# Kernel optimization log

Hardware: AMD Instinct MI355X
Metric: run time of the kernel (lower is better)

## Reference

```python
import jax, jax.numpy as jnp
import numpy as np
from jax import lax

NUM_HEADS = 8
HEAD_DIM = 32
DIM = NUM_HEADS * HEAD_DIM  # 256
SR = 2
B, H, W = 4, 64, 64


def setup_inputs() -> dict:
    key = jax.random.key(0)
    ks = jax.random.split(key, 6)
    x = jax.random.normal(ks[0], (B, DIM, H, W), dtype=jnp.float32)
    # query: 1x1 conv without bias -> plain [out,in] matrix
    Wq = jax.random.normal(ks[1], (DIM, DIM), dtype=jnp.float32) * (1.0 / np.sqrt(DIM))
    # key/value: sr x sr conv, stride sr, no bias (OIHW)
    Wk = jax.random.normal(ks[2], (DIM, DIM, SR, SR), dtype=jnp.float32) * (1.0 / np.sqrt(DIM * SR * SR))
    Wv = jax.random.normal(ks[3], (DIM, DIM, SR, SR), dtype=jnp.float32) * (1.0 / np.sqrt(DIM * SR * SR))
    rel_h = jax.random.normal(ks[4], (1, NUM_HEADS, HEAD_DIM, 1, H // SR), dtype=jnp.float32)
    rel_w = jax.random.normal(ks[5], (1, NUM_HEADS, HEAD_DIM, W // SR, 1), dtype=jnp.float32)
    return {"x": x, "Wq": Wq, "Wk": Wk, "Wv": Wv, "rel_h": rel_h, "rel_w": rel_w}


def reference(x, Wq, Wk, Wv, rel_h, rel_w):
    b, c, h, w = x.shape
    nh, hd = NUM_HEADS, HEAD_DIM
    scale = hd ** (-0.5)
    dn = ('NCHW', 'OIHW', 'NCHW')

    # q: 1x1 conv == channel matmul; [B, C, H*W] -> [B, nh, hd, Nq]
    q = jnp.einsum('oc,bchw->bohw', Wq, x).reshape(b, nh, hd, h * w)
    # k, v: sr x sr conv, stride sr -> [B, nh, hd, Nkv]
    k = lax.conv_general_dilated(x, Wk, window_strides=(SR, SR), padding='VALID',
                                 dimension_numbers=dn).reshape(b, nh, hd, -1)
    v = lax.conv_general_dilated(x, Wv, window_strides=(SR, SR), padding='VALID',
                                 dimension_numbers=dn).reshape(b, nh, hd, -1)

    # attn scores: q^T k -> [B, nh, Nq, Nkv]
    attn = jnp.einsum('bhdn,bhdm->bhnm', q, k)
    # relative positional bias: (rel_h + rel_w) broadcast -> [nh, hd, Nkv]
    pos = (rel_h + rel_w).reshape(nh, hd, -1)
    attn = attn + jnp.einsum('bhdn,hdm->bhnm', q, pos)
    attn = jax.nn.softmax(attn * scale, axis=-1)

    # out = v @ attn^T -> [B, nh, hd, Nq] -> [B, C, H, W]
    out = jnp.einsum('bhdm,bhnm->bhdn', v, attn).reshape(b, c, h, w)
    return out
```

## Files before the change

kernel.cpp:

```cpp
#include <hip/hip_runtime.h>
#include <math.h>


typedef __bf16 bf16;
typedef __attribute__((ext_vector_type(8))) __bf16 bf16x8;
typedef __attribute__((ext_vector_type(4))) float f32x4;
typedef __attribute__((ext_vector_type(4))) _Float16 f16x4;

#define MFMA16 __builtin_amdgcn_mfma_f32_16x16x32_bf16
#define MFMA16H __builtin_amdgcn_mfma_f32_16x16x16f16

#define QSCALE 0.25503486f
#define SOFTMAX_SHIFT 10.0f

__global__ void k_prep_w(const float* __restrict__ Wq, const float* __restrict__ Wk,
                         const float* __restrict__ Wv,
                         bf16* __restrict__ Wq_bf, bf16* __restrict__ Wkv_bf) {
    int idx = blockIdx.x * 256 + threadIdx.x;
    Wq_bf[idx] = (bf16)(Wq[idx] * QSCALE);
#pragma unroll
    for (int r = 0; r < 8; r++) {
        int e = idx + r * 65536;
        int c = e >> 10, kk = e & 1023;
        int tap = kk >> 8, i = kk & 255;
        const float* Wsrc = (c < 256) ? Wk : Wv;
        int cs = c & 255;
        Wkv_bf[e] = (bf16)Wsrc[(cs * 256 + i) * 4 + tap];
    }
}

__global__ void k_xT(const float* __restrict__ x, bf16* __restrict__ xT) {
    int b = blockIdx.z, c0 = blockIdx.y * 64, n0 = blockIdx.x * 64;
    __shared__ float tile[64][65];
    int t = threadIdx.x;
    const float* xp = x + (size_t)(b * 256 + c0) * 4096 + n0;
#pragma unroll
    for (int k2 = 0; k2 < 16; k2++) {
        int flat = k2 * 256 + t;
        int row = flat >> 6, col = flat & 63;
        tile[row][col] = xp[(size_t)row * 4096 + col];
    }
    __syncthreads();
    bf16* op = xT + (size_t)(b * 4096 + n0) * 256 + c0;
#pragma unroll
    for (int k2 = 0; k2 < 16; k2++) {
        int flat = k2 * 256 + t;
        int row = flat >> 6, col = flat & 63;
        op[(size_t)row * 256 + col] = (bf16)tile[col][row];
    }
}

__launch_bounds__(256)
__global__ void k_gemm_q(const bf16* __restrict__ xT, const bf16* __restrict__ Wq_bf,
                         bf16* __restrict__ q_t) {
    int b = blockIdx.z;
    int n0 = blockIdx.x * 64, c0 = blockIdx.y * 64;
    int t = threadIdx.x, l = t & 63, w = t >> 6;
    int wn = (w & 1) * 32, wc = (w >> 1) * 32;
    int lr = l & 15, lg = l >> 4;
    const bf16* Ab = xT + (size_t)(b * 4096 + n0 + wn + lr) * 256 + lg * 8;
    const bf16* Bb = Wq_bf + (size_t)(c0 + wc + lr) * 256 + lg * 8;
    f32x4 acc[2][2] = {};
#pragma unroll
    for (int kk = 0; kk < 8; kk++) {
        bf16x8 a0 = *(const bf16x8*)(Ab + kk * 32);
        bf16x8 a1 = *(const bf16x8*)(Ab + 16 * 256 + kk * 32);
        bf16x8 b0 = *(const bf16x8*)(Bb + kk * 32);
        bf16x8 b1 = *(const bf16x8*)(Bb + 16 * 256 + kk * 32);
        acc[0][0] = MFMA16(a0, b0, acc[0][0], 0, 0, 0);
        acc[0][1] = MFMA16(a0, b1, acc[0][1], 0, 0, 0);
        acc[1][0] = MFMA16(a1, b0, acc[1][0], 0, 0, 0);
        acc[1][1] = MFMA16(a1, b1, acc[1][1], 0, 0, 0);
    }
#pragma unroll
    for (int i = 0; i < 2; i++)
#pragma unroll
        for (int j = 0; j < 2; j++) {
            int cc = c0 + wc + j * 16 + lr;
            int h = cc >> 5, d = cc & 31;
#pragma unroll
            for (int r = 0; r < 4; r++) {
                int n = n0 + wn + i * 16 + lg * 4 + r;
                q_t[((size_t)(b * 8 + h) * 4096 + n) * 32 + d] = (bf16)acc[i][j][r];
            }
        }
}

__device__ inline void p_row_ptrs(const bf16* __restrict__ xb, int m, int lgofs,
                                  const bf16* __restrict__ p[4]) {
    int y = m >> 5, xw = m & 31;
    int nb = y * 128 + xw * 2;
#pragma unroll
    for (int tap = 0; tap < 4; tap++) {
        int n = nb + (tap >> 1) * 64 + (tap & 1);
        p[tap] = xb + (size_t)n * 256 + lgofs;
    }
}
__device__ inline void c_row_ptrs(const bf16* __restrict__ row, int lgofs,
                                  const bf16* __restrict__ p[4]) {
#pragma unroll
    for (int tap = 0; tap < 4; tap++) p[tap] = row + tap * 256 + lgofs;
}

__launch_bounds__(256)
__global__ void k_gemm_kv(const bf16* __restrict__ xT, const bf16* __restrict__ Wkv_bf,
                          const float* __restrict__ rel_h, const float* __restrict__ rel_w,
                          bf16* __restrict__ kpos_t, _Float16* __restrict__ v_td) {
    int b = blockIdx.z;
    int m0 = blockIdx.x * 64;
    int zz = blockIdx.y;
    bool vmode = zz >= 4;
    int c0 = (zz & 3) * 64;
    int t = threadIdx.x, l = t & 63, w = t >> 6;
    int wr = (w & 1) * 32, wc = (w >> 1) * 32;
    int lr = l & 15, lg = l >> 4;
    int lgofs = lg * 8;
    const bf16* xb = xT + (size_t)b * 4096 * 256;
    const bf16 *A0[4], *A1[4], *B0[4], *B1[4];
    if (!vmode) {
        p_row_ptrs(xb, m0 + wr + lr, lgofs, A0);
        p_row_ptrs(xb, m0 + wr + 16 + lr, lgofs, A1);
        c_row_ptrs(Wkv_bf + (size_t)(c0 + wc + lr) * 1024, lgofs, B0);
        c_row_ptrs(Wkv_bf + (size_t)(c0 + wc + 16 + lr) * 1024, lgofs, B1);
    } else {
        c_row_ptrs(Wkv_bf + (size_t)(256 + c0 + wr + lr) * 1024, lgofs, A0);
        c_row_ptrs(Wkv_bf + (size_t)(256 + c0 + wr + 16 + lr) * 1024, lgofs, A1);
        p_row_ptrs(xb, m0 + wc + lr, lgofs, B0);
        p_row_ptrs(xb, m0 + wc + 16 + lr, lgofs, B1);
    }
    f32x4 acc[2][2] = {};
#pragma unroll
    for (int tap = 0; tap < 4; tap++) {
#pragma unroll
        for (int j = 0; j < 8; j++) {
            int o = j * 32;
            bf16x8 a0 = *(const bf16x8*)(A0[tap] + o);
            bf16x8 a1 = *(const bf16x8*)(A1[tap] + o);
            bf16x8 b0 = *(const bf16x8*)(B0[tap] + o);
            bf16x8 b1 = *(const bf16x8*)(B1[tap] + o);
            acc[0][0] = MFMA16(a0, b0, acc[0][0], 0, 0, 0);
            acc[0][1] = MFMA16(a0, b1, acc[0][1], 0, 0, 0);
            acc[1][0] = MFMA16(a1, b0, acc[1][0], 0, 0, 0);
            acc[1][1] = MFMA16(a1, b1, acc[1][1], 0, 0, 0);
        }
    }
    if (!vmode) {
#pragma unroll
        for (int i = 0; i < 2; i++)
#pragma unroll
            for (int j = 0; j < 2; j++) {
                int cc = c0 + wc + j * 16 + lr;
#pragma unroll
                for (int r = 0; r < 4; r++) {
                    int m = m0 + wr + i * 16 + lg * 4 + r;
                    float val = acc[i][j][r] + rel_w[cc * 32 + (m >> 5)]
                                            + rel_h[cc * 32 + (m & 31)];
                    kpos_t[((size_t)(b * 8 + (cc >> 5)) * 1024 + m) * 32 + (cc & 31)] = (bf16)val;
                }
            }
    } else {
#pragma unroll
        for (int i = 0; i < 2; i++)
#pragma unroll
            for (int j = 0; j < 2; j++) {
                int m = m0 + wc + j * 16 + lr;
#pragma unroll
                for (int r = 0; r < 4; r++) {
                    int cc = c0 + wr + i * 16 + lg * 4 + r;
                    v_td[((size_t)(b * 8 + (cc >> 5)) * 32 + (cc & 31)) * 1024 + m] = (_Float16)acc[i][j][r];
                }
            }
    }
}

__launch_bounds__(256)
__global__ void k_attn(const bf16* __restrict__ q_t, const bf16* __restrict__ kpos_t,
                       const _Float16* __restrict__ v_td, float* __restrict__ out) {
    int b = blockIdx.z, h = blockIdx.y;
    int t = threadIdx.x;
    int w = t >> 6, l = t & 63;
    int n0 = blockIdx.x * 128 + w * 32;
    int lr = l & 15, lg = l >> 4;
    const size_t bh = (size_t)(b * 8 + h);
    __shared__ __align__(16) bf16 Ks[256 * 32];
    __shared__ __align__(16) _Float16 Vs[32][264];
    bf16x8 bq0 = *(const bf16x8*)(q_t + (bh * 4096 + n0 + lr) * 32 + lg * 8);
    bf16x8 bq1 = *(const bf16x8*)(q_t + (bh * 4096 + n0 + 16 + lr) * 32 + lg * 8);
    const bf16* Kb = kpos_t + bh * 1024 * 32;
    const _Float16* Vb = v_td + bh * 32 * 1024;
    f32x4 accO[2][2] = {};
    float ps0 = 0.f, ps1 = 0.f;
    const f32x4 zs = {-SOFTMAX_SHIFT, -SOFTMAX_SHIFT, -SOFTMAX_SHIFT, -SOFTMAX_SHIFT};
    for (int pass = 0; pass < 4; pass++) {
        const uint4* ksrc = (const uint4*)(Kb + (size_t)pass * 256 * 32);
        uint4* kdst = (uint4*)Ks;
#pragma unroll
        for (int j = 0; j < 4; j++) kdst[t + j * 256] = ksrc[t + j * 256];
#pragma unroll
        for (int j = 0; j < 4; j++) {
            int u = t + j * 256;
            int row = u >> 5, col = u & 31;
            *(uint4*)(&Vs[row][col * 8]) =
                *(const uint4*)(Vb + (size_t)row * 1024 + pass * 256 + col * 8);
        }
        __syncthreads();
#pragma unroll 4
        for (int tt = 0; tt < 16; tt++) {
            bf16x8 ak = *(const bf16x8*)(Ks + (tt * 16 + lr) * 32 + lg * 8);
            f32x4 s0 = MFMA16(ak, bq0, zs, 0, 0, 0);
            f32x4 s1 = MFMA16(ak, bq1, zs, 0, 0, 0);
            f16x4 p0, p1;
#pragma unroll
            for (int r = 0; r < 4; r++) {
                float e0 = fminf(__builtin_amdgcn_exp2f(s0[r]), 65504.f);
                float e1 = fminf(__builtin_amdgcn_exp2f(s1[r]), 65504.f);
                ps0 += e0; ps1 += e1;
                p0[r] = (_Float16)e0; p1[r] = (_Float16)e1;
            }
            f16x4 v0 = *(const f16x4*)(&Vs[lr][tt * 16 + lg * 4]);
            f16x4 v1 = *(const f16x4*)(&Vs[16 + lr][tt * 16 + lg * 4]);
            accO[0][0] = MFMA16H(p0, v0, accO[0][0], 0, 0, 0);
            accO[0][1] = MFMA16H(p0, v1, accO[0][1], 0, 0, 0);
            accO[1][0] = MFMA16H(p1, v0, accO[1][0], 0, 0, 0);
            accO[1][1] = MFMA16H(p1, v1, accO[1][1], 0, 0, 0);
        }
        __syncthreads();
    }
    ps0 += __shfl_xor(ps0, 16, 64); ps0 += __shfl_xor(ps0, 32, 64);
    ps1 += __shfl_xor(ps1, 16, 64); ps1 += __shfl_xor(ps1, 32, 64);
    float inv0[4], inv1[4];
#pragma unroll
    for (int r = 0; r < 4; r++) {
        inv0[r] = 1.0f / __shfl(ps0, lg * 4 + r, 64);
        inv1[r] = 1.0f / __shfl(ps1, lg * 4 + r, 64);
    }
#pragma unroll
    for (int dt = 0; dt < 2; dt++) {
        int c = h * 32 + dt * 16 + lr;
        float* op0 = out + (size_t)(b * 256 + c) * 4096 + n0 + lg * 4;
        float* op1 = op0 + 16;
        f32x4 o0, o1;
#pragma unroll
        for (int r = 0; r < 4; r++) {
            o0[r] = accO[0][dt][r] * inv0[r];
            o1[r] = accO[1][dt][r] * inv1[r];
        }
        *(f32x4*)op0 = o0;
        *(f32x4*)op1 = o1;
    }
}

extern "C" void kernel_launch(void* const* d_in, const int* in_sizes, int n_in,
                              void* d_out, int out_size, void* d_ws, size_t ws_size,
                              hipStream_t stream) {
    const float* x    = (const float*)d_in[0];
    const float* Wq   = (const float*)d_in[1];
    const float* Wk   = (const float*)d_in[2];
    const float* Wv   = (const float*)d_in[3];
    const float* relh = (const float*)d_in[4];
    const float* relw = (const float*)d_in[5];
    float* out = (float*)d_out;
    char* ws = (char*)d_ws;

    bf16*      xT     = (bf16*)(ws);
    bf16*      q_t    = (bf16*)(ws + (8u << 20));
    bf16*      kposT  = (bf16*)(ws + (16u << 20));
    _Float16*  v_td   = (_Float16*)(ws + (18u << 20));
    bf16*      Wq_bf  = (bf16*)(ws + (20u << 20));
    bf16*      Wkv_bf = (bf16*)(ws + (20u << 20) + (256u << 10));

    k_prep_w <<<256,            256, 0, stream>>>(Wq, Wk, Wv, Wq_bf, Wkv_bf);
    k_xT     <<<dim3(64, 4, 4), 256, 0, stream>>>(x, xT);
    k_gemm_q <<<dim3(64, 4, 4), 256, 0, stream>>>(xT, Wq_bf, q_t);
    k_gemm_kv<<<dim3(16, 8, 4), 256, 0, stream>>>(xT, Wkv_bf, relh, relw, kposT, v_td);
    k_attn   <<<dim3(32, 8, 4), 256, 0, stream>>>(q_t, kposT, v_td, out);
}
```

Before: 170.0 us.

## Fuse Q projection into attention kernel and shrink KV GEMM tiles

```diff
diff --git a/kernel.cpp b/kernel.cpp
--- a/kernel.cpp
+++ b/kernel.cpp
@@ -50,42 +50,6 @@
     }
 }
 
-__launch_bounds__(256)
-__global__ void k_gemm_q(const bf16* __restrict__ xT, const bf16* __restrict__ Wq_bf,
-                         bf16* __restrict__ q_t) {
-    int b = blockIdx.z;
-    int n0 = blockIdx.x * 64, c0 = blockIdx.y * 64;
-    int t = threadIdx.x, l = t & 63, w = t >> 6;
-    int wn = (w & 1) * 32, wc = (w >> 1) * 32;
-    int lr = l & 15, lg = l >> 4;
-    const bf16* Ab = xT + (size_t)(b * 4096 + n0 + wn + lr) * 256 + lg * 8;
-    const bf16* Bb = Wq_bf + (size_t)(c0 + wc + lr) * 256 + lg * 8;
-    f32x4 acc[2][2] = {};
-#pragma unroll
-    for (int kk = 0; kk < 8; kk++) {
-        bf16x8 a0 = *(const bf16x8*)(Ab + kk * 32);
-        bf16x8 a1 = *(const bf16x8*)(Ab + 16 * 256 + kk * 32);
-        bf16x8 b0 = *(const bf16x8*)(Bb + kk * 32);
-        bf16x8 b1 = *(const bf16x8*)(Bb + 16 * 256 + kk * 32);
-        acc[0][0] = MFMA16(a0, b0, acc[0][0], 0, 0, 0);
-        acc[0][1] = MFMA16(a0, b1, acc[0][1], 0, 0, 0);
-        acc[1][0] = MFMA16(a1, b0, acc[1][0], 0, 0, 0);
-        acc[1][1] = MFMA16(a1, b1, acc[1][1], 0, 0, 0);
-    }
-#pragma unroll
-    for (int i = 0; i < 2; i++)
-#pragma unroll
-        for (int j = 0; j < 2; j++) {
-            int cc = c0 + wc + j * 16 + lr;
-            int h = cc >> 5, d = cc & 31;
-#pragma unroll
-            for (int r = 0; r < 4; r++) {
-                int n = n0 + wn + i * 16 + lg * 4 + r;
-                q_t[((size_t)(b * 8 + h) * 4096 + n) * 32 + d] = (bf16)acc[i][j][r];
-            }
-        }
-}
-
 __device__ inline void p_row_ptrs(const bf16* __restrict__ xb, int m, int lgofs,
                                   const bf16* __restrict__ p[4]) {
     int y = m >> 5, xw = m & 31;
@@ -107,75 +71,75 @@
                           const float* __restrict__ rel_h, const float* __restrict__ rel_w,
                           bf16* __restrict__ kpos_t, _Float16* __restrict__ v_td) {
     int b = blockIdx.z;
-    int m0 = blockIdx.x * 64;
+    int m0 = blockIdx.x * 32;
     int zz = blockIdx.y;
     bool vmode = zz >= 4;
     int c0 = (zz & 3) * 64;
     int t = threadIdx.x, l = t & 63, w = t >> 6;
-    int wr = (w & 1) * 32, wc = (w >> 1) * 32;
     int lr = l & 15, lg = l >> 4;
     int lgofs = lg * 8;
     const bf16* xb = xT + (size_t)b * 4096 * 256;
-    const bf16 *A0[4], *A1[4], *B0[4], *B1[4];
+    const bf16 *F0[4], *F1[4], *G0[4];
     if (!vmode) {
-        p_row_ptrs(xb, m0 + wr + lr, lgofs, A0);
-        p_row_ptrs(xb, m0 + wr + 16 + lr, lgofs, A1);
-        c_row_ptrs(Wkv_bf + (size_t)(c0 + wc + lr) * 1024, lgofs, B0);
-        c_row_ptrs(Wkv_bf + (size_t)(c0 + wc + 16 + lr) * 1024, lgofs, B1);
+        p_row_ptrs(xb, m0 + lr, lgofs, F0);
+        p_row_ptrs(xb, m0 + 16 + lr, lgofs, F1);
+        c_row_ptrs(Wkv_bf + (size_t)(c0 + w * 16 + lr) * 1024, lgofs, G0);
     } else {
-        c_row_ptrs(Wkv_bf + (size_t)(256 + c0 + wr + lr) * 1024, lgofs, A0);
-        c_row_ptrs(Wkv_bf + (size_t)(256 + c0 + wr + 16 + lr) * 1024, lgofs, A1);
-        p_row_ptrs(xb, m0 + wc + lr, lgofs, B0);
-        p_row_ptrs(xb, m0 + wc + 16 + lr, lgofs, B1);
-    }
-    f32x4 acc[2][2] = {};
-#pragma unroll
-    for (int tap = 0; tap < 4; tap++) {
-#pragma unroll
-        for (int j = 0; j < 8; j++) {
-            int o = j * 32;
-            bf16x8 a0 = *(const bf16x8*)(A0[tap] + o);
-            bf16x8 a1 = *(const bf16x8*)(A1[tap] + o);
-            bf16x8 b0 = *(const bf16x8*)(B0[tap] + o);
-            bf16x8 b1 = *(const bf16x8*)(B1[tap] + o);
-            acc[0][0] = MFMA16(a0, b0, acc[0][0], 0, 0, 0);
-            acc[0][1] = MFMA16(a0, b1, acc[0][1], 0, 0, 0);
-            acc[1][0] = MFMA16(a1, b0, acc[1][0], 0, 0, 0);
-            acc[1][1] = MFMA16(a1, b1, acc[1][1], 0, 0, 0);
-        }
-    }
+        c_row_ptrs(Wkv_bf + (size_t)(256 + c0 + w * 16 + lr) * 1024, lgofs, G0);
+        p_row_ptrs(xb, m0 + lr, lgofs, F0);
+        p_row_ptrs(xb, m0 + 16 + lr, lgofs, F1);
+    }
+    f32x4 acc[2] = {};
     if (!vmode) {
 #pragma unroll
+        for (int tap = 0; tap < 4; tap++)
+#pragma unroll
+            for (int j = 0; j < 8; j++) {
+                int o = j * 32;
+                bf16x8 a0 = *(const bf16x8*)(F0[tap] + o);
+                bf16x8 a1 = *(const bf16x8*)(F1[tap] + o);
+                bf16x8 b0 = *(const bf16x8*)(G0[tap] + o);
+                acc[0] = MFMA16(a0, b0, acc[0], 0, 0, 0);
+                acc[1] = MFMA16(a1, b0, acc[1], 0, 0, 0);
+            }
+        int cc = c0 + w * 16 + lr;
+#pragma unroll
         for (int i = 0; i < 2; i++)
 #pragma unroll
-            for (int j = 0; j < 2; j++) {
-                int cc = c0 + wc + j * 16 + lr;
-#pragma unroll
-                for (int r = 0; r < 4; r++) {
-                    int m = m0 + wr + i * 16 + lg * 4 + r;
-                    float val = acc[i][j][r] + rel_w[cc * 32 + (m >> 5)]
-                                            + rel_h[cc * 32 + (m & 31)];
-                    kpos_t[((size_t)(b * 8 + (cc >> 5)) * 1024 + m) * 32 + (cc & 31)] = (bf16)val;
-                }
+            for (int r = 0; r < 4; r++) {
+                int m = m0 + i * 16 + lg * 4 + r;
+                float val = acc[i][r] + rel_w[cc * 32 + (m >> 5)]
+                                      + rel_h[cc * 32 + (m & 31)];
+                kpos_t[((size_t)(b * 8 + (cc >> 5)) * 1024 + m) * 32 + (cc & 31)] = (bf16)val;
             }
     } else {
 #pragma unroll
-        for (int i = 0; i < 2; i++)
-#pragma unroll
-            for (int j = 0; j < 2; j++) {
-                int m = m0 + wc + j * 16 + lr;
-#pragma unroll
-                for (int r = 0; r < 4; r++) {
-                    int cc = c0 + wr + i * 16 + lg * 4 + r;
-                    v_td[((size_t)(b * 8 + (cc >> 5)) * 32 + (cc & 31)) * 1024 + m] = (_Float16)acc[i][j][r];
-                }
-            }
+        for (int tap = 0; tap < 4; tap++)
+#pragma unroll
+            for (int j = 0; j < 8; j++) {
+                int o = j * 32;
+                bf16x8 a0 = *(const bf16x8*)(G0[tap] + o);
+                bf16x8 b0 = *(const bf16x8*)(F0[tap] + o);
+                bf16x8 b1 = *(const bf16x8*)(F1[tap] + o);
+                acc[0] = MFMA16(a0, b0, acc[0], 0, 0, 0);
+                acc[1] = MFMA16(a0, b1, acc[1], 0, 0, 0);
+            }
+#pragma unroll
+        for (int j = 0; j < 2; j++) {
+            int m = m0 + j * 16 + lr;
+#pragma unroll
+            for (int r = 0; r < 4; r++) {
+                int cc = c0 + w * 16 + lg * 4 + r;
+                v_td[((size_t)(b * 8 + (cc >> 5)) * 32 + (cc & 31)) * 1024 + m] = (_Float16)acc[j][r];
+            }
+        }
     }
 }
 
 __launch_bounds__(256)
-__global__ void k_attn(const bf16* __restrict__ q_t, const bf16* __restrict__ kpos_t,
-                       const _Float16* __restrict__ v_td, float* __restrict__ out) {
+__global__ void k_attn(const bf16* __restrict__ xT, const bf16* __restrict__ Wq_bf,
+                       const bf16* __restrict__ kpos_t, const _Float16* __restrict__ v_td,
+                       float* __restrict__ out) {
     int b = blockIdx.z, h = blockIdx.y;
     int t = threadIdx.x;
     int w = t >> 6, l = t & 63;
@@ -184,8 +148,33 @@
     const size_t bh = (size_t)(b * 8 + h);
     __shared__ __align__(16) bf16 Ks[256 * 32];
     __shared__ __align__(16) _Float16 Vs[32][264];
-    bf16x8 bq0 = *(const bf16x8*)(q_t + (bh * 4096 + n0 + lr) * 32 + lg * 8);
-    bf16x8 bq1 = *(const bf16x8*)(q_t + (bh * 4096 + n0 + 16 + lr) * 32 + lg * 8);
+    bf16* Qs = Ks + w * 1024;
+    {
+        const bf16* Aw = Wq_bf + (size_t)(h * 32 + lr) * 256 + lg * 8;
+        const bf16* Bx = xT + (size_t)(b * 4096 + n0 + lr) * 256 + lg * 8;
+        f32x4 aq[2][2] = {};
+#pragma unroll
+        for (int kk = 0; kk < 8; kk++) {
+            bf16x8 a0 = *(const bf16x8*)(Aw + kk * 32);
+            bf16x8 a1 = *(const bf16x8*)(Aw + 16 * 256 + kk * 32);
+            bf16x8 b0 = *(const bf16x8*)(Bx + kk * 32);
+            bf16x8 b1 = *(const bf16x8*)(Bx + 16 * 256 + kk * 32);
+            aq[0][0] = MFMA16(a0, b0, aq[0][0], 0, 0, 0);
+            aq[0][1] = MFMA16(a0, b1, aq[0][1], 0, 0, 0);
+            aq[1][0] = MFMA16(a1, b0, aq[1][0], 0, 0, 0);
+            aq[1][1] = MFMA16(a1, b1, aq[1][1], 0, 0, 0);
+        }
+#pragma unroll
+        for (int i = 0; i < 2; i++)
+#pragma unroll
+            for (int j = 0; j < 2; j++)
+#pragma unroll
+                for (int r = 0; r < 4; r++)
+                    Qs[(j * 16 + lr) * 32 + i * 16 + lg * 4 + r] = (bf16)aq[i][j][r];
+    }
+    bf16x8 bq0 = *(const bf16x8*)(Qs + lr * 32 + lg * 8);
+    bf16x8 bq1 = *(const bf16x8*)(Qs + (16 + lr) * 32 + lg * 8);
+    __syncthreads();
     const bf16* Kb = kpos_t + bh * 1024 * 32;
     const _Float16* Vb = v_td + bh * 32 * 1024;
     f32x4 accO[2][2] = {};
@@ -263,15 +252,13 @@
     char* ws = (char*)d_ws;
 
     bf16*      xT     = (bf16*)(ws);
-    bf16*      q_t    = (bf16*)(ws + (8u << 20));
-    bf16*      kposT  = (bf16*)(ws + (16u << 20));
-    _Float16*  v_td   = (_Float16*)(ws + (18u << 20));
-    bf16*      Wq_bf  = (bf16*)(ws + (20u << 20));
-    bf16*      Wkv_bf = (bf16*)(ws + (20u << 20) + (256u << 10));
+    bf16*      kposT  = (bf16*)(ws + (8u << 20));
+    _Float16*  v_td   = (_Float16*)(ws + (10u << 20));
+    bf16*      Wq_bf  = (bf16*)(ws + (12u << 20));
+    bf16*      Wkv_bf = (bf16*)(ws + (12u << 20) + (256u << 10));
 
     k_prep_w <<<256,            256, 0, stream>>>(Wq, Wk, Wv, Wq_bf, Wkv_bf);
     k_xT     <<<dim3(64, 4, 4), 256, 0, stream>>>(x, xT);
-    k_gemm_q <<<dim3(64, 4, 4), 256, 0, stream>>>(xT, Wq_bf, q_t);
-    k_gemm_kv<<<dim3(16, 8, 4), 256, 0, stream>>>(xT, Wkv_bf, relh, relw, kposT, v_td);
-    k_attn   <<<dim3(32, 8, 4), 256, 0, stream>>>(q_t, kposT, v_td, out);
-}
+    k_gemm_kv<<<dim3(32, 8, 4), 256, 0, stream>>>(xT, Wkv_bf, relh, relw, kposT, v_td);
+    k_attn   <<<dim3(32, 8, 4), 256, 0, stream>>>(xT, Wq_bf, kposT, v_td, out);
+}
```

New measurement: 177.6 us. +4.5%, slower.
